# Kernel tuning notes

Hardware: AMD Instinct MI355X
Metric: run time of the kernel (lower is better)

The kernel has to match this reference:

```python
import jax, jax.numpy as jnp
import numpy as np

N_NODES = 50000
N_EDGES = 640000
IN_C, HID_C, OUT_C = 64, 128, 64


def _glorot(key, fan_in, fan_out):
    lim = float(np.sqrt(6.0 / (fan_in + fan_out)))
    return jax.random.uniform(key, (fan_in, fan_out), jnp.float32, -lim, lim)


def setup_inputs() -> dict:
    key = jax.random.key(0)
    ks = jax.random.split(key, 16)
    x = jax.random.normal(ks[0], (N_NODES, IN_C), jnp.float32)
    edge_index = jax.random.randint(ks[1], (2, N_EDGES), 0, N_NODES, jnp.int64)
    # SAGEConv params: out = mean_aggr(x_j) @ Wl + x @ Wr + b
    dims = [(IN_C, HID_C), (HID_C, HID_C), (HID_C, OUT_C)]
    params = {}
    for i, (fi, fo) in enumerate(dims):
        params[f"Wl{i}"] = _glorot(ks[2 + 3 * i], fi, fo)
        params[f"Wr{i}"] = _glorot(ks[3 + 3 * i], fi, fo)
        params[f"b{i}"] = jnp.zeros((fo,), jnp.float32)
    # classifier: Linear(64,32) -> ReLU -> Linear(32,1) -> Sigmoid (dropout off in eval)
    params["Wc1"] = _glorot(ks[11], OUT_C, 32)
    params["bc1"] = jnp.zeros((32,), jnp.float32)
    params["Wc2"] = _glorot(ks[12], 32, 1)
    params["bc2"] = jnp.zeros((1,), jnp.float32)
    return {"x": x, "edge_index": edge_index, **params}


def _sage_conv(x, src, dst, Wl, Wr, b):
    # gather neighbor (source) features along edges, mean-aggregate at target
    msgs = x[src]                                                    # [E, C]
    agg = jax.ops.segment_sum(msgs, dst, num_segments=N_NODES)      # [N, C]
    deg = jax.ops.segment_sum(jnp.ones((src.shape[0], 1), x.dtype), dst,
                              num_segments=N_NODES)                 # [N, 1]
    agg = agg / jnp.maximum(deg, 1.0)
    return agg @ Wl + x @ Wr + b


def reference(x, edge_index, Wl0, Wr0, b0, Wl1, Wr1, b1, Wl2, Wr2, b2,
              Wc1, bc1, Wc2, bc2):
    src, dst = edge_index[0], edge_index[1]
    h = jax.nn.relu(_sage_conv(x, src, dst, Wl0, Wr0, b0))
    h = jax.nn.relu(_sage_conv(h, src, dst, Wl1, Wr1, b1))
    h = _sage_conv(h, src, dst, Wl2, Wr2, b2)                       # [N, 64]
    h = jax.nn.relu(h @ Wc1 + bc1)                                  # [N, 32]
    return jax.nn.sigmoid(h @ Wc2 + bc2)                            # [N, 1]
```

## Files before the change

### kernel.cpp

```cpp
#include <hip/hip_runtime.h>
#include <hip/hip_cooperative_groups.h>
#include <math.h>

namespace cg = cooperative_groups;

#define NN 50000
#define NE 640000
#define CAP 64

typedef short short8 __attribute__((ext_vector_type(8)));
typedef float f32x4  __attribute__((ext_vector_type(4)));

__device__ __forceinline__ unsigned bfr(float f) {
    unsigned u = __float_as_uint(f);
    return (u + 0x7FFFu + ((u >> 16) & 1u)) >> 16;
}
__device__ __forceinline__ unsigned pk2(float a, float b) { return bfr(a) | (bfr(b) << 16); }
__device__ __forceinline__ float bflo(unsigned u) { return __uint_as_float(u << 16); }
__device__ __forceinline__ float bfhi(unsigned u) { return __uint_as_float(u & 0xFFFF0000u); }

__device__ __forceinline__ void packOne(const float* Wl, const float* Wr,
                                        unsigned short* wp, int idx,
                                        int CIN, int COUT) {
    int k = idx / COUT, n = idx % COUT;
    float v = (k < CIN) ? Wl[k * COUT + n] : Wr[(k - CIN) * COUT + n];
    int kt = k >> 5, quad = (k >> 3) & 3, j = k & 7;
    int nt = n >> 4, l16 = n & 15;
    int NT = COUT / 16;
    wp[(((kt * NT + nt) * 64) + quad * 16 + l16) * 8 + j] = (unsigned short)bfr(v);
}

template <int LOGC>
__device__ __forceinline__ void
agg_phase(const unsigned* __restrict__ xu, const int* __restrict__ nbr,
          const int* __restrict__ cnt, unsigned* __restrict__ aggu,
          int wgl, int nwave, int lane) {
    constexpr int RU = 1 << (LOGC - 1);
    constexpr int PC = RU / 16;
    const int qw = lane >> 4, l16 = lane & 15;

    for (int gw = wgl; gw < NN; gw += nwave) {
        const int deg = cnt[gw];
        const int m = (deg < CAP) ? deg : CAP;

        int idx = 0;
        if (lane < m) idx = nbr[gw * CAP + lane];

        float a[2 * PC] = {};

#pragma unroll 4
        for (int j = 0; j < m; j += 4) {
            const int n = __shfl(idx, (j + qw) & 63);
            const bool valid = (j + qw) < m;
            if (PC == 2) {
                const uint2 u = *(const uint2*)(xu + (size_t)n * RU + l16 * 2);
                if (valid) {
                    a[0] += bflo(u.x); a[1] += bfhi(u.x);
                    a[2] += bflo(u.y); a[3] += bfhi(u.y);
                }
            } else {
                const uint4 u = *(const uint4*)(xu + (size_t)n * RU + l16 * 4);
                if (valid) {
                    a[0] += bflo(u.x); a[1] += bfhi(u.x);
                    a[2] += bflo(u.y); a[3] += bfhi(u.y);
                    a[4] += bflo(u.z); a[5] += bfhi(u.z);
                    a[6] += bflo(u.w); a[7] += bfhi(u.w);
                }
            }
        }

#pragma unroll
        for (int c = 0; c < 2 * PC; ++c) {
            a[c] += __shfl_xor(a[c], 16);
            a[c] += __shfl_xor(a[c], 32);
        }

        if (qw == 0) {
            const float di = 1.0f / (float)((deg > 1) ? deg : 1);
            if (PC == 2) {
                uint2 o = make_uint2(pk2(a[0] * di, a[1] * di), pk2(a[2] * di, a[3] * di));
                *(uint2*)(aggu + (size_t)gw * RU + l16 * 2) = o;
            } else {
                uint4 o = make_uint4(pk2(a[0] * di, a[1] * di), pk2(a[2] * di, a[3] * di),
                                     pk2(a[4] * di, a[5] * di), pk2(a[6] * di, a[7] * di));
                *(uint4*)(aggu + (size_t)gw * RU + l16 * 4) = o;
            }
        }
    }
}

template <int CIN, int COUT, bool RELU>
__device__ __forceinline__ void
mfma_phase(const unsigned short* __restrict__ Agg, const unsigned short* __restrict__ X,
           const unsigned short* __restrict__ Wpack, const float* __restrict__ bias,
           unsigned short* __restrict__ outp, int blk, int gstride, int wave, int lane) {
    constexpr int KT = (2 * CIN) / 32;
    constexpr int NT = COUT / 16;
    const int quad = lane >> 4, l16 = lane & 15;
    const int NTILE = (NN + 127) / 128;

    for (int tile = blk; tile < NTILE; tile += gstride) {
        const int row_base = tile * 128 + wave * 32;
        int r0 = row_base + l16;      if (r0 >= NN) r0 = NN - 1;
        int r1 = row_base + 16 + l16; if (r1 >= NN) r1 = NN - 1;

        f32x4 acc[2][NT] = {};

        for (int kt = 0; kt < KT; ++kt) {
            const unsigned short* P = (kt < KT / 2) ? Agg : X;
            const int kb = (kt < KT / 2) ? kt * 32 : kt * 32 - CIN;
            const short8 a0 = *(const short8*)(P + (size_t)r0 * CIN + kb + quad * 8);
            const short8 a1 = *(const short8*)(P + (size_t)r1 * CIN + kb + quad * 8);
#pragma unroll
            for (int nt = 0; nt < NT; ++nt) {
                const short8 bfrag = *(const short8*)(Wpack + (size_t)((kt * NT + nt) * 64 + lane) * 8);
                acc[0][nt] = __builtin_amdgcn_mfma_f32_16x16x32_bf16(a0, bfrag, acc[0][nt], 0, 0, 0);
                acc[1][nt] = __builtin_amdgcn_mfma_f32_16x16x32_bf16(a1, bfrag, acc[1][nt], 0, 0, 0);
            }
        }

#pragma unroll
        for (int nt = 0; nt < NT; ++nt) {
            const int col = nt * 16 + l16;
            const float bb = bias[col];
#pragma unroll
            for (int s = 0; s < 2; ++s) {
#pragma unroll
                for (int rg = 0; rg < 4; ++rg) {
                    int row = row_base + s * 16 + quad * 4 + rg;
                    if (row < NN) {
                        float v = acc[s][nt][rg] + bb;
                        if (RELU) v = fmaxf(v, 0.f);
                        outp[(size_t)row * COUT + col] = (unsigned short)bfr(v);
                    }
                }
            }
        }
    }
}

__global__ __launch_bounds__(256) void
k_all(const int* __restrict__ src, const int* __restrict__ dst,
      const float* __restrict__ x,
      const float* Wl0, const float* Wr0, const float* b0,
      const float* Wl1, const float* Wr1, const float* b1,
      const float* Wl2, const float* Wr2, const float* b2,
      const float* Wc1, const float* bc1, const float* Wc2, const float* bc2,
      int* cnt, int* nbr, unsigned short* xb,
      unsigned short* wp0, unsigned short* wp1, unsigned short* wp2,
      unsigned short* wpc,
      unsigned short* aggb, unsigned short* h0b, unsigned short* h1b,
      float* out) {
    cg::grid_group grid = cg::this_grid();

    __shared__ __align__(16) short Hs[8 * 16 * 64];

    const int t = threadIdx.x, b = blockIdx.x;
    const int nthr = gridDim.x * 256;
    const int nwave = nthr >> 6;
    const int gt = b * 256 + t;
    const int wave = t >> 6, lane = t & 63;
    const int wgl = gt >> 6;
    const int quad = lane >> 4, l16 = lane & 15;

    for (int e = gt; e < NE; e += nthr) {
        int d = dst[e];
        int p = atomicAdd(&cnt[d], 1);
        if (p < CAP) nbr[d * CAP + p] = src[e];
    }
    for (int i = gt; i < NN * 16; i += nthr) {
        float4 v = ((const float4*)x)[i];
        ((uint2*)xb)[i] = make_uint2(pk2(v.x, v.y), pk2(v.z, v.w));
    }
    for (int i = gt; i < 67584; i += nthr) {
        if (i < 16384) packOne(Wl0, Wr0, wp0, i, 64, 128);
        else if (i < 49152) packOne(Wl1, Wr1, wp1, i - 16384, 128, 128);
        else if (i < 65536) packOne(Wl2, Wr2, wp2, i - 49152, 128, 64);
        else packOne(Wc1, Wc1, wpc, i - 65536, 64, 32);
    }
    grid.sync();

    agg_phase<6>((const unsigned*)xb, nbr, cnt, (unsigned*)aggb, wgl, nwave, lane);
    grid.sync();
    mfma_phase<64, 128, true>(aggb, xb, wp0, b0, h0b, b, gridDim.x, wave, lane);
    grid.sync();

    agg_phase<7>((const unsigned*)h0b, nbr, cnt, (unsigned*)aggb, wgl, nwave, lane);
    grid.sync();
    mfma_phase<128, 128, true>(aggb, h0b, wp1, b1, h1b, b, gridDim.x, wave, lane);
    grid.sync();

    agg_phase<7>((const unsigned*)h1b, nbr, cnt, (unsigned*)aggb, wgl, nwave, lane);
    grid.sync();

    {
        constexpr int CIN = 128, NT = 4, KT = 8;
        const int NTILE = (NN + 127) / 128;

        for (int tile = b; tile < NTILE; tile += gridDim.x) {
            const int row_base = tile * 128 + wave * 32;
            int r0 = row_base + l16;      if (r0 >= NN) r0 = NN - 1;
            int r1 = row_base + 16 + l16; if (r1 >= NN) r1 = NN - 1;

            f32x4 acc[2][NT] = {};

            for (int kt = 0; kt < KT; ++kt) {
                const unsigned short* P = (kt < KT / 2) ? aggb : h1b;
                const int kb = (kt < KT / 2) ? kt * 32 : kt * 32 - CIN;
                const short8 a0 = *(const short8*)(P + (size_t)r0 * CIN + kb + quad * 8);
                const short8 a1 = *(const short8*)(P + (size_t)r1 * CIN + kb + quad * 8);
#pragma unroll
                for (int nt = 0; nt < NT; ++nt) {
                    const short8 bfrag = *(const short8*)(wp2 + (size_t)((kt * NT + nt) * 64 + lane) * 8);
                    acc[0][nt] = __builtin_amdgcn_mfma_f32_16x16x32_bf16(a0, bfrag, acc[0][nt], 0, 0, 0);
                    acc[1][nt] = __builtin_amdgcn_mfma_f32_16x16x32_bf16(a1, bfrag, acc[1][nt], 0, 0, 0);
                }
            }

#pragma unroll
            for (int nt = 0; nt < NT; ++nt) {
                const float bb = b2[nt * 16 + l16];
#pragma unroll
                for (int s = 0; s < 2; ++s)
#pragma unroll
                    for (int rg = 0; rg < 4; ++rg)
                        Hs[(wave * 2 + s) * 1024 + (quad * 4 + rg) * 64 + nt * 16 + l16] =
                            (unsigned short)bfr(acc[s][nt][rg] + bb);
            }
            __syncthreads();

            f32x4 sacc[2][2] = {};
#pragma unroll
            for (int s = 0; s < 2; ++s)
#pragma unroll
                for (int kt2 = 0; kt2 < 2; ++kt2) {
                    const short8 af = *(const short8*)&Hs[(wave * 2 + s) * 1024 + l16 * 64 +
                                                          kt2 * 32 + quad * 8];
#pragma unroll
                    for (int nt2 = 0; nt2 < 2; ++nt2) {
                        const short8 bf = *(const short8*)(wpc + (size_t)((kt2 * 2 + nt2) * 64 + lane) * 8);
                        sacc[s][nt2] = __builtin_amdgcn_mfma_f32_16x16x32_bf16(af, bf, sacc[s][nt2], 0, 0, 0);
                    }
                }

            const float b1a = bc1[l16], b1b = bc1[16 + l16];
            const float w2a = Wc2[l16], w2b = Wc2[16 + l16];
            const float b2v = bc2[0];
#pragma unroll
            for (int s = 0; s < 2; ++s)
#pragma unroll
                for (int rg = 0; rg < 4; ++rg) {
                    float p = fmaxf(sacc[s][0][rg] + b1a, 0.f) * w2a +
                              fmaxf(sacc[s][1][rg] + b1b, 0.f) * w2b;
#pragma unroll
                    for (int off = 1; off < 16; off <<= 1) p += __shfl_xor(p, off);
                    if (l16 == 0) {
                        int row = row_base + s * 16 + quad * 4 + rg;
                        if (row < NN) out[row] = 1.0f / (1.0f + expf(-(p + b2v)));
                    }
                }
            __syncthreads();
        }
    }
}

__global__ __launch_bounds__(256) void
k_prep(const int* __restrict__ src, const int* __restrict__ dst,
       int* __restrict__ cnt, int* __restrict__ nbr,
       const float* __restrict__ x, unsigned* __restrict__ xb,
       const float* Wl0, const float* Wr0, const float* Wl1, const float* Wr1,
       const float* Wl2, const float* Wr2, const float* Wc1,
       unsigned short* wp0, unsigned short* wp1, unsigned short* wp2,
       unsigned short* wpc) {
    const int b = blockIdx.x, t = threadIdx.x;
    if (b < 2500) {
        int e = b * 256 + t;
        if (e < NE) {
            int d = dst[e];
            int p = atomicAdd(&cnt[d], 1);
            if (p < CAP) nbr[d * CAP + p] = src[e];
        }
    } else if (b < 5625) {
        int i = (b - 2500) * 256 + t;
        if (i < NN * 16) {
            float4 v = ((const float4*)x)[i];
            ((uint2*)xb)[i] = make_uint2(pk2(v.x, v.y), pk2(v.z, v.w));
        }
    } else {
        int idx = (b - 5625) * 256 + t;
        if (idx < 16384) packOne(Wl0, Wr0, wp0, idx, 64, 128);
        else if (idx < 49152) packOne(Wl1, Wr1, wp1, idx - 16384, 128, 128);
        else if (idx < 65536) packOne(Wl2, Wr2, wp2, idx - 49152, 128, 64);
        else if (idx < 67584) packOne(Wc1, Wc1, wpc, idx - 65536, 64, 32);
    }
}

template <int LOGC>
__global__ __launch_bounds__(256) void
k_aggregate(const unsigned* __restrict__ xu, const int* __restrict__ nbr,
            const int* __restrict__ cnt, unsigned* __restrict__ aggu, int N) {
    const int wgl = (blockIdx.x * 256 + threadIdx.x) >> 6;
    if (wgl >= N) return;
    agg_phase<LOGC>(xu, nbr, cnt, aggu, wgl, 1 << 30, threadIdx.x & 63);
}

template <int CIN, int COUT, bool RELU>
__global__ __launch_bounds__(256) void
k_mfma(const unsigned short* __restrict__ Agg, const unsigned short* __restrict__ X,
       const unsigned short* __restrict__ Wpack, const float* __restrict__ bias,
       unsigned short* __restrict__ outp, int N) {
    mfma_phase<CIN, COUT, RELU>(Agg, X, Wpack, bias, outp,
                                blockIdx.x, 1 << 30, threadIdx.x >> 6, threadIdx.x & 63);
}

__global__ __launch_bounds__(256) void
k_mfma_cls(const unsigned short* __restrict__ Agg, const unsigned short* __restrict__ X,
           const unsigned short* __restrict__ Wpack, const unsigned short* __restrict__ WpackC,
           const float* __restrict__ bias, const float* __restrict__ bc1,
           const float* __restrict__ Wc2, const float* __restrict__ bc2,
           float* __restrict__ out, int N) {
    constexpr int CIN = 128, NT = 4, KT = 8;

    __shared__ __align__(16) short Hs[8 * 16 * 64];

    const int t = threadIdx.x;
    const int wave = t >> 6, lane = t & 63;
    const int quad = lane >> 4, l16 = lane & 15;

    const int row_base = blockIdx.x * 128 + wave * 32;
    int r0 = row_base + l16;      if (r0 >= N) r0 = N - 1;
    int r1 = row_base + 16 + l16; if (r1 >= N) r1 = N - 1;

    f32x4 acc[2][NT] = {};

    for (int kt = 0; kt < KT; ++kt) {
        const unsigned short* P = (kt < KT / 2) ? Agg : X;
        const int kb = (kt < KT / 2) ? kt * 32 : kt * 32 - CIN;
        const short8 a0 = *(const short8*)(P + (size_t)r0 * CIN + kb + quad * 8);
        const short8 a1 = *(const short8*)(P + (size_t)r1 * CIN + kb + quad * 8);
#pragma unroll
        for (int nt = 0; nt < NT; ++nt) {
            const short8 bfrag = *(const short8*)(Wpack + (size_t)((kt * NT + nt) * 64 + lane) * 8);
            acc[0][nt] = __builtin_amdgcn_mfma_f32_16x16x32_bf16(a0, bfrag, acc[0][nt], 0, 0, 0);
            acc[1][nt] = __builtin_amdgcn_mfma_f32_16x16x32_bf16(a1, bfrag, acc[1][nt], 0, 0, 0);
        }
    }

#pragma unroll
    for (int nt = 0; nt < NT; ++nt) {
        const float bb = bias[nt * 16 + l16];
#pragma unroll
        for (int s = 0; s < 2; ++s)
#pragma unroll
            for (int rg = 0; rg < 4; ++rg)
                Hs[(wave * 2 + s) * 1024 + (quad * 4 + rg) * 64 + nt * 16 + l16] =
                    (unsigned short)bfr(acc[s][nt][rg] + bb);
    }
    __syncthreads();

    f32x4 sacc[2][2] = {};
#pragma unroll
    for (int s = 0; s < 2; ++s)
#pragma unroll
        for (int kt2 = 0; kt2 < 2; ++kt2) {
            const short8 af = *(const short8*)&Hs[(wave * 2 + s) * 1024 + l16 * 64 +
                                                  kt2 * 32 + quad * 8];
#pragma unroll
            for (int nt2 = 0; nt2 < 2; ++nt2) {
                const short8 bf = *(const short8*)(WpackC + (size_t)((kt2 * 2 + nt2) * 64 + lane) * 8);
                sacc[s][nt2] = __builtin_amdgcn_mfma_f32_16x16x32_bf16(af, bf, sacc[s][nt2], 0, 0, 0);
            }
        }

    const float b1a = bc1[l16], b1b = bc1[16 + l16];
    const float w2a = Wc2[l16], w2b = Wc2[16 + l16];
    const float b2v = bc2[0];
#pragma unroll
    for (int s = 0; s < 2; ++s)
#pragma unroll
        for (int rg = 0; rg < 4; ++rg) {
            float p = fmaxf(sacc[s][0][rg] + b1a, 0.f) * w2a +
                      fmaxf(sacc[s][1][rg] + b1b, 0.f) * w2b;
#pragma unroll
            for (int off = 1; off < 16; off <<= 1) p += __shfl_xor(p, off);
            if (l16 == 0) {
                int row = row_base + s * 16 + quad * 4 + rg;
                if (row < N) out[row] = 1.0f / (1.0f + expf(-(p + b2v)));
            }
        }
}

extern "C" void kernel_launch(void* const* d_in, const int* in_sizes, int n_in,
                              void* d_out, int out_size, void* d_ws, size_t ws_size,
                              hipStream_t stream) {
    const float* x   = (const float*)d_in[0];
    const int*   ei  = (const int*)d_in[1];
    const int*   src = ei;
    const int*   dst = ei + NE;
    const float* Wl0 = (const float*)d_in[2];
    const float* Wr0 = (const float*)d_in[3];
    const float* b0  = (const float*)d_in[4];
    const float* Wl1 = (const float*)d_in[5];
    const float* Wr1 = (const float*)d_in[6];
    const float* b1  = (const float*)d_in[7];
    const float* Wl2 = (const float*)d_in[8];
    const float* Wr2 = (const float*)d_in[9];
    const float* b2  = (const float*)d_in[10];
    const float* Wc1 = (const float*)d_in[11];
    const float* bc1 = (const float*)d_in[12];
    const float* Wc2 = (const float*)d_in[13];
    const float* bc2 = (const float*)d_in[14];
    float* out = (float*)d_out;

    char*  ws   = (char*)d_ws;
    int*   cnt  = (int*)(ws);
    unsigned short* wp0 = (unsigned short*)(ws + (size_t)256 * 1024);
    unsigned short* wp1 = (unsigned short*)(ws + (size_t)352 * 1024);
    unsigned short* wp2 = (unsigned short*)(ws + (size_t)448 * 1024);
    unsigned short* wpc = (unsigned short*)(ws + (size_t)512 * 1024);
    int*   nbr  = (int*)(ws + (size_t)1 * (1 << 20));
    unsigned short* xb   = (unsigned short*)(ws + (size_t)16 * (1 << 20));
    unsigned short* aggb = (unsigned short*)(ws + (size_t)24 * (1 << 20));
    unsigned short* h0b  = (unsigned short*)(ws + (size_t)40 * (1 << 20));
    unsigned short* h1b  = (unsigned short*)(ws + (size_t)56 * (1 << 20));

    hipMemsetAsync(cnt, 0, (size_t)NN * sizeof(int), stream);

    bool coop_ok = false;
    int maxBpc = 0, ncu = 0, dev = 0;
    hipGetDevice(&dev);
    hipDeviceGetAttribute(&ncu, hipDeviceAttributeMultiprocessorCount, dev);
    hipError_t qerr = hipOccupancyMaxActiveBlocksPerMultiprocessor(
        &maxBpc, (const void*)k_all, 256, 0);
    if (qerr == hipSuccess && maxBpc > 0 && ncu > 0) {
        int grid = maxBpc * ncu;
        if (grid > 2048) grid = 2048;
        const int* srcp = src; const int* dstp = dst;
        void* args[] = {
            (void*)&srcp, (void*)&dstp, (void*)&x,
            (void*)&Wl0, (void*)&Wr0, (void*)&b0,
            (void*)&Wl1, (void*)&Wr1, (void*)&b1,
            (void*)&Wl2, (void*)&Wr2, (void*)&b2,
            (void*)&Wc1, (void*)&bc1, (void*)&Wc2, (void*)&bc2,
            (void*)&cnt, (void*)&nbr, (void*)&xb,
            (void*)&wp0, (void*)&wp1, (void*)&wp2, (void*)&wpc,
            (void*)&aggb, (void*)&h0b, (void*)&h1b,
            (void*)&out
        };
        hipError_t lerr = hipLaunchCooperativeKernel((const void*)k_all, dim3(grid),
                                                     dim3(256), args, 0, stream);
        if (lerr == hipSuccess) coop_ok = true;
        else (void)hipGetLastError();
    } else {
        (void)hipGetLastError();
    }

    if (!coop_ok) {
        const int B = 256;
        const int AGG_GRID = (NN + 3) / 4;
        const int MFMA_GRID = (NN + 127) / 128;

        k_prep<<<5889, B, 0, stream>>>(src, dst, cnt, nbr, x, (unsigned*)xb,
                                       Wl0, Wr0, Wl1, Wr1, Wl2, Wr2, Wc1,
                                       wp0, wp1, wp2, wpc);

        k_aggregate<6><<<AGG_GRID, B, 0, stream>>>((const unsigned*)xb, nbr, cnt,
                                                   (unsigned*)aggb, NN);
        k_mfma<64, 128, true><<<MFMA_GRID, B, 0, stream>>>(aggb, xb, wp0, b0, h0b, NN);

        k_aggregate<7><<<AGG_GRID, B, 0, stream>>>((const unsigned*)h0b, nbr, cnt,
                                                   (unsigned*)aggb, NN);
        k_mfma<128, 128, true><<<MFMA_GRID, B, 0, stream>>>(aggb, h0b, wp1, b1, h1b, NN);

        k_aggregate<7><<<AGG_GRID, B, 0, stream>>>((const unsigned*)h1b, nbr, cnt,
                                                   (unsigned*)aggb, NN);
        k_mfma_cls<<<MFMA_GRID, B, 0, stream>>>(aggb, h1b, wp2, wpc, b2, bc1, Wc2, bc2,
                                                out, NN);
    }
}
```

Before: 235.2 us.

## Aggregate each node with a 16-lane group and use a zero pad row

The mean-aggregation phase now assigns one 16-lane group per node instead of a full 64-lane wave, so each wave handles four nodes at once. Neighbor indices are loaded 16 at a time and broadcast with width-16 shuffles. Missing slots point at an extra zero row at index NN of each feature buffer, which removes per-load predication and the cross-quad shuffle reduction. The cost is up to 15 wasted (cached) loads per node when degree is not a multiple of 16. It also depends on the feature buffers having room for that extra row.

```diff
diff --git a/kernel.cpp b/kernel.cpp
--- a/kernel.cpp
+++ b/kernel.cpp
@@ -34,33 +34,28 @@
 __device__ __forceinline__ void
 agg_phase(const unsigned* __restrict__ xu, const int* __restrict__ nbr,
           const int* __restrict__ cnt, unsigned* __restrict__ aggu,
-          int wgl, int nwave, int lane) {
+          int gid, int ngroups, int l16) {
     constexpr int RU = 1 << (LOGC - 1);
     constexpr int PC = RU / 16;
-    const int qw = lane >> 4, l16 = lane & 15;
-
-    for (int gw = wgl; gw < NN; gw += nwave) {
+
+    for (int gw = gid; gw < NN; gw += ngroups) {
         const int deg = cnt[gw];
         const int m = (deg < CAP) ? deg : CAP;
 
-        int idx = 0;
-        if (lane < m) idx = nbr[gw * CAP + lane];
-
         float a[2 * PC] = {};
 
-#pragma unroll 4
-        for (int j = 0; j < m; j += 4) {
-            const int n = __shfl(idx, (j + qw) & 63);
-            const bool valid = (j + qw) < m;
-            if (PC == 2) {
-                const uint2 u = *(const uint2*)(xu + (size_t)n * RU + l16 * 2);
-                if (valid) {
+        for (int base = 0; base < m; base += 16) {
+            int idx = NN;
+            if (base + l16 < m) idx = nbr[gw * CAP + base + l16];
+#pragma unroll
+            for (int j = 0; j < 16; ++j) {
+                const int n = __shfl(idx, j, 16);
+                if (PC == 2) {
+                    const uint2 u = *(const uint2*)(xu + (size_t)n * RU + l16 * 2);
                     a[0] += bflo(u.x); a[1] += bfhi(u.x);
                     a[2] += bflo(u.y); a[3] += bfhi(u.y);
-                }
-            } else {
-                const uint4 u = *(const uint4*)(xu + (size_t)n * RU + l16 * 4);
-                if (valid) {
+                } else {
+                    const uint4 u = *(const uint4*)(xu + (size_t)n * RU + l16 * 4);
                     a[0] += bflo(u.x); a[1] += bfhi(u.x);
                     a[2] += bflo(u.y); a[3] += bfhi(u.y);
                     a[4] += bflo(u.z); a[5] += bfhi(u.z);
@@ -69,22 +64,14 @@
             }
         }
 
-#pragma unroll
-        for (int c = 0; c < 2 * PC; ++c) {
-            a[c] += __shfl_xor(a[c], 16);
-            a[c] += __shfl_xor(a[c], 32);
-        }
-
-        if (qw == 0) {
-            const float di = 1.0f / (float)((deg > 1) ? deg : 1);
-            if (PC == 2) {
-                uint2 o = make_uint2(pk2(a[0] * di, a[1] * di), pk2(a[2] * di, a[3] * di));
-                *(uint2*)(aggu + (size_t)gw * RU + l16 * 2) = o;
-            } else {
-                uint4 o = make_uint4(pk2(a[0] * di, a[1] * di), pk2(a[2] * di, a[3] * di),
-                                     pk2(a[4] * di, a[5] * di), pk2(a[6] * di, a[7] * di));
-                *(uint4*)(aggu + (size_t)gw * RU + l16 * 4) = o;
-            }
+        const float di = 1.0f / (float)((deg > 1) ? deg : 1);
+        if (PC == 2) {
+            uint2 o = make_uint2(pk2(a[0] * di, a[1] * di), pk2(a[2] * di, a[3] * di));
+            *(uint2*)(aggu + (size_t)gw * RU + l16 * 2) = o;
+        } else {
+            uint4 o = make_uint4(pk2(a[0] * di, a[1] * di), pk2(a[2] * di, a[3] * di),
+                                 pk2(a[4] * di, a[5] * di), pk2(a[6] * di, a[7] * di));
+            *(uint4*)(aggu + (size_t)gw * RU + l16 * 4) = o;
         }
     }
 }
@@ -157,11 +144,11 @@
 
     const int t = threadIdx.x, b = blockIdx.x;
     const int nthr = gridDim.x * 256;
-    const int nwave = nthr >> 6;
     const int gt = b * 256 + t;
     const int wave = t >> 6, lane = t & 63;
-    const int wgl = gt >> 6;
     const int quad = lane >> 4, l16 = lane & 15;
+    const int gid = gt >> 4;
+    const int ngroups = nthr >> 4;
 
     for (int e = gt; e < NE; e += nthr) {
         int d = dst[e];
@@ -172,6 +159,9 @@
         float4 v = ((const float4*)x)[i];
         ((uint2*)xb)[i] = make_uint2(pk2(v.x, v.y), pk2(v.z, v.w));
     }
+    if (gt < 32) ((unsigned*)xb)[(size_t)NN * 32 + gt] = 0u;
+    else if (gt < 96) ((unsigned*)h0b)[(size_t)NN * 64 + (gt - 32)] = 0u;
+    else if (gt < 160) ((unsigned*)h1b)[(size_t)NN * 64 + (gt - 96)] = 0u;
     for (int i = gt; i < 67584; i += nthr) {
         if (i < 16384) packOne(Wl0, Wr0, wp0, i, 64, 128);
         else if (i < 49152) packOne(Wl1, Wr1, wp1, i - 16384, 128, 128);
@@ -180,17 +170,17 @@
     }
     grid.sync();
 
-    agg_phase<6>((const unsigned*)xb, nbr, cnt, (unsigned*)aggb, wgl, nwave, lane);
+    agg_phase<6>((const unsigned*)xb, nbr, cnt, (unsigned*)aggb, gid, ngroups, t & 15);
     grid.sync();
     mfma_phase<64, 128, true>(aggb, xb, wp0, b0, h0b, b, gridDim.x, wave, lane);
     grid.sync();
 
-    agg_phase<7>((const unsigned*)h0b, nbr, cnt, (unsigned*)aggb, wgl, nwave, lane);
+    agg_phase<7>((const unsigned*)h0b, nbr, cnt, (unsigned*)aggb, gid, ngroups, t & 15);
     grid.sync();
     mfma_phase<128, 128, true>(aggb, h0b, wp1, b1, h1b, b, gridDim.x, wave, lane);
     grid.sync();
 
-    agg_phase<7>((const unsigned*)h1b, nbr, cnt, (unsigned*)aggb, wgl, nwave, lane);
+    agg_phase<7>((const unsigned*)h1b, nbr, cnt, (unsigned*)aggb, gid, ngroups, t & 15);
     grid.sync();
 
     {
@@ -271,7 +261,7 @@
        const float* Wl0, const float* Wr0, const float* Wl1, const float* Wr1,
        const float* Wl2, const float* Wr2, const float* Wc1,
        unsigned short* wp0, unsigned short* wp1, unsigned short* wp2,
-       unsigned short* wpc) {
+       unsigned short* wpc, unsigned short* h0b, unsigned short* h1b) {
     const int b = blockIdx.x, t = threadIdx.x;
     if (b < 2500) {
         int e = b * 256 + t;
@@ -280,6 +270,11 @@
             int p = atomicAdd(&cnt[d], 1);
             if (p < CAP) nbr[d * CAP + p] = src[e];
         }
+        if (b == 0) {
+            if (t < 32) xb[(size_t)NN * 32 + t] = 0u;
+            else if (t < 96) ((unsigned*)h0b)[(size_t)NN * 64 + (t - 32)] = 0u;
+            else if (t < 160) ((unsigned*)h1b)[(size_t)NN * 64 + (t - 96)] = 0u;
+        }
     } else if (b < 5625) {
         int i = (b - 2500) * 256 + t;
         if (i < NN * 16) {
@@ -299,9 +294,9 @@
 __global__ __launch_bounds__(256) void
 k_aggregate(const unsigned* __restrict__ xu, const int* __restrict__ nbr,
             const int* __restrict__ cnt, unsigned* __restrict__ aggu, int N) {
-    const int wgl = (blockIdx.x * 256 + threadIdx.x) >> 6;
-    if (wgl >= N) return;
-    agg_phase<LOGC>(xu, nbr, cnt, aggu, wgl, 1 << 30, threadIdx.x & 63);
+    const int gid = (blockIdx.x * 256 + threadIdx.x) >> 4;
+    if (gid >= N) return;
+    agg_phase<LOGC>(xu, nbr, cnt, aggu, gid, 1 << 30, threadIdx.x & 15);
 }
 
 template <int CIN, int COUT, bool RELU>
@@ -457,12 +452,12 @@
 
     if (!coop_ok) {
         const int B = 256;
-        const int AGG_GRID = (NN + 3) / 4;
+        const int AGG_GRID = (NN * 16 + 255) / 256;
         const int MFMA_GRID = (NN + 127) / 128;
 
         k_prep<<<5889, B, 0, stream>>>(src, dst, cnt, nbr, x, (unsigned*)xb,
                                        Wl0, Wr0, Wl1, Wr1, Wl2, Wr2, Wc1,
-                                       wp0, wp1, wp2, wpc);
+                                       wp0, wp1, wp2, wpc, h0b, h1b);
 
         k_aggregate<6><<<AGG_GRID, B, 0, stream>>>((const unsigned*)xb, nbr, cnt,
                                                    (unsigned*)aggb, NN);
```

New measurement: 239.1 us. About the same (+1.6%).
